# Performance work log

Measured on AMD Instinct MI355X. Metric: run time of the kernel, lower is better.

The kernel has to match this reference:

```python
import jax, jax.numpy as jnp
import numpy as np


def _sig_gram(X, Y, n):
    """Signature-kernel gram matrix via the Goursat PDE recurrence.
    X: (A, M, D), Y: (B, N, D). Returns (A, B) of k(x_a, y_b).
    Recurrence: K[i+1,j+1] = K[i+1,j] + K[i,j+1] + K[i,j]*(inc_ij - 1).
    """
    f = 2 ** n
    # dyadic refinement: increments scaled by 1/2^n, each repeated 2^n times
    dX = jnp.repeat((X[:, 1:] - X[:, :-1]) / f, f, axis=1)  # (A, Mg-1, D)
    dY = jnp.repeat((Y[:, 1:] - Y[:, :-1]) / f, f, axis=1)  # (B, Ng-1, D)
    inc = jnp.einsum('aid,bjd->abij', dX, dY)               # (A, B, Mg-1, Ng-1)
    A, B, _, Ng1 = inc.shape
    ones_col = jnp.ones((A, B, 1), inc.dtype)

    def row_step(K_prev, inc_row):
        # K_prev: row i of the PDE grid, shape (A,B,Ng1+1); inc_row: (A,B,Ng1)
        diag = K_prev[..., :-1] * (inc_row - 1.0)  # K[i,j]*inc - K[i,j]
        up = K_prev[..., 1:]                        # K[i,j+1]

        def col_step(k_left, uv):
            u, d = uv
            k = k_left + u + d
            return k, k

        _, krow = jax.lax.scan(
            col_step,
            jnp.ones((A, B), inc.dtype),
            (jnp.moveaxis(up, -1, 0), jnp.moveaxis(diag, -1, 0)),
        )
        K_new = jnp.concatenate([ones_col, jnp.moveaxis(krow, 0, -1)], axis=-1)
        return K_new, None

    K0 = jnp.ones((A, B, Ng1 + 1), inc.dtype)  # boundary row K[0,:] = 1
    K_last, _ = jax.lax.scan(row_step, K0, jnp.moveaxis(inc, 2, 0))
    return K_last[..., -1]  # K[-1,-1] for every pair


def setup_inputs() -> dict:
    key = jax.random.key(0)
    kx, ky = jax.random.split(key)
    SCALE = 0.05  # keep kernel values in fp32 range (exponential growth)
    X = jax.random.normal(kx, (64, 128, 16), dtype=jnp.float32) * SCALE
    Y = jax.random.normal(ky, (64, 128, 16), dtype=jnp.float32) * SCALE
    return {"X": X, "Y": Y, "n": 0}


def reference(X, Y, n):
    k_xx = _sig_gram(X, X, n)
    k_yy = _sig_gram(Y, Y, n)
    k_xy = _sig_gram(X, Y, n)
    return jnp.mean(k_xx) + jnp.mean(k_yy) - 2.0 * jnp.mean(k_xy)
```

## Files before the change

kernel.cpp:

```cpp
#include <hip/hip_runtime.h>


#define DINC_PER 130048
#define XY_BLOCKS 1024
#define TRI_BLOCKS 544
#define NBT (XY_BLOCKS + 2 * TRI_BLOCKS)
#define NBLOCKS4 2048

template <int C, int RM, int BM, bool BC>
__device__ __forceinline__ float dpp0(float x) {
    return __builtin_bit_cast(float, __builtin_amdgcn_update_dpp(
        0, __builtin_bit_cast(int, x), C, RM, BM, BC));
}

__device__ __forceinline__ float wave_scan_incl(float v) {
    v += dpp0<0x111, 0xf, 0xf, true>(v);
    v += dpp0<0x112, 0xf, 0xf, true>(v);
    v += dpp0<0x114, 0xf, 0xf, true>(v);
    v += dpp0<0x118, 0xf, 0xf, true>(v);
    v += dpp0<0x142, 0xa, 0xf, false>(v);
    v += dpp0<0x143, 0xc, 0xf, false>(v);
    return v;
}

__device__ __forceinline__ float wave_shr1(float x, float oldv) {
    return __builtin_bit_cast(float, __builtin_amdgcn_update_dpp(
        __builtin_bit_cast(int, oldv), __builtin_bit_cast(int, x),
        0x138, 0xf, 0xf, false));
}

__global__ __launch_bounds__(256) void sig_diff(
    const float* __restrict__ X, const float* __restrict__ Y,
    float* __restrict__ dInc, float* __restrict__ out)
{
    if (blockIdx.x == 0 && threadIdx.x == 0) out[0] = 0.0f;
    int i = blockIdx.x * 256 + threadIdx.x;
    if (i >= 65024) return;
    int which = (i >= 32512) ? 1 : 0;
    int j = i - which * 32512;
    int a = j / 508;
    int rq = j - a * 508;
    const float* S = which ? Y : X;
    const float4* p = (const float4*)(S + a * 2048) + rq;
    float4 v0 = p[0], v1 = p[4];
    float4 d;
    d.x = v1.x - v0.x; d.y = v1.y - v0.y;
    d.z = v1.z - v0.z; d.w = v1.w - v0.w;
    ((float4*)dInc)[i] = d;
}

__global__ __launch_bounds__(256, 4) void sig_pde4(
    const float* __restrict__ dInc, float* __restrict__ out)
{
    __shared__ float red[4];
    const int wid  = threadIdx.x >> 6;
    const int lane = threadIdx.x & 63;

    float acc = 0.0f;
    const int nt = (blockIdx.x < (NBT - NBLOCKS4)) ? 2 : 1;

#pragma unroll 1
    for (int it = 0; it < nt; ++it) {
        const int BT = it ? (int)(NBLOCKS4 + blockIdx.x) : (int)blockIdx.x;

        int g, a, b0;
        if (BT < XY_BLOCKS) {
            g = 2; a = BT >> 4; b0 = (BT & 15) << 2;
        } else {
            int t = BT - XY_BLOCKS; g = 0;
            if (t >= TRI_BLOCKS) { t -= TRI_BLOCKS; g = 1; }
            int aa = 0;
            for (;;) { int nb = (67 - aa) >> 2; if (t < nb) break; t -= nb; ++aa; }
            a = aa; b0 = aa + (t << 2);
        }
        const int b = b0 + wid;

        if (g == 2 || b <= 63) {
            const float* dA = (g == 1) ? (dInc + DINC_PER) : dInc;
            const float* dB = (g == 0) ? dInc : (dInc + DINC_PER);
            const float weight = (g == 2) ? (-2.0f / 4096.0f)
                                          : ((a == b ? 1.0f : 2.0f) / 4096.0f);

            float ya[16], yb_[16];
            {
                const float* Qb = dB + b * 2032;
                const int j0 = lane << 1;
                const int j1 = (j0 + 1 < 127) ? j0 + 1 : 126;
                const float4* A4 = (const float4*)(Qb + j0 * 16);
                const float4* B4 = (const float4*)(Qb + j1 * 16);
#pragma unroll
                for (int q = 0; q < 4; ++q) {
                    float4 va = A4[q], vb = B4[q];
                    ya[4*q+0]=va.x;  ya[4*q+1]=va.y;  ya[4*q+2]=va.z;  ya[4*q+3]=va.w;
                    yb_[4*q+0]=vb.x; yb_[4*q+1]=vb.y; yb_[4*q+2]=vb.z; yb_[4*q+3]=vb.w;
                }
            }
#pragma unroll
            for (int d = 0; d < 16; ++d)
                asm volatile("" : "+v"(ya[d]), "+v"(yb_[d]));

            const int abase = __builtin_amdgcn_readfirstlane(a * 2032);
            const float4* Ar = (const float4*)(dA + abase);

            float xr[16], xn[16];
#pragma unroll
            for (int q = 0; q < 4; ++q) {
                float4 v = Ar[q];
                xr[4*q+0]=v.x; xr[4*q+1]=v.y; xr[4*q+2]=v.z; xr[4*q+3]=v.w;
            }

            float g_lo = 1.0f, g_hi = 1.0f;
            const bool last = (lane == 63);

#define SIG_ROW(XROW)                                                       \
            {                                                               \
                float s0=-0.5f, s1=-0.5f, t0=-0.5f, t1=-0.5f;               \
                _Pragma("unroll")                                           \
                for (int d = 0; d < 16; d += 2) {                           \
                    s0 = fmaf(XROW[d],   ya[d],    s0);                     \
                    s1 = fmaf(XROW[d+1], ya[d+1],  s1);                     \
                    t0 = fmaf(XROW[d],   yb_[d],   t0);                     \
                    t1 = fmaf(XROW[d+1], yb_[d+1], t1);                     \
                }                                                           \
                const float i0 = s0 + s1;             \
                const float i1 = t0 + t1;             \
                const float gl = wave_shr1(g_hi, 1.0f);       \
                const float c0 = fmaf(gl, i0, g_lo);                        \
                const float c1 = last ? 0.0f : fmaf(g_lo, i1, g_hi);        \
                const float S  = wave_scan_incl(c0 + c1);                   \
                g_lo = (S - c1) + 1.0f;                                     \
                g_hi = S + 1.0f;                                            \
            }

#pragma unroll 1
            for (int r = 0; r < 126; r += 2) {
#pragma unroll
                for (int q = 0; q < 4; ++q) {
                    float4 v = Ar[4*(r+1)+q];
                    xn[4*q+0]=v.x; xn[4*q+1]=v.y; xn[4*q+2]=v.z; xn[4*q+3]=v.w;
                }
                SIG_ROW(xr)
#pragma unroll
                for (int q = 0; q < 4; ++q) {
                    float4 v = Ar[4*(r+2)+q];
                    xr[4*q+0]=v.x; xr[4*q+1]=v.y; xr[4*q+2]=v.z; xr[4*q+3]=v.w;
                }
                SIG_ROW(xn)
            }
            SIG_ROW(xr)
#undef SIG_ROW

            const float kab = __builtin_bit_cast(float,
                __builtin_amdgcn_readlane(__builtin_bit_cast(int, g_lo), 63));
            acc = fmaf(weight, kab, acc);
        }
    }

    if (lane == 0) red[wid] = acc;
    __syncthreads();
    if (threadIdx.x == 0)
        atomicAdd(out, (red[0] + red[1]) + (red[2] + red[3]));
}

__global__ __launch_bounds__(256) void sig_reduce2(
    const float* __restrict__ v, float* __restrict__ out, int n)
{
    __shared__ float red[256];
    float s = 0.0f;
    for (int i = threadIdx.x; i < n; i += 256) s += v[i];
    red[threadIdx.x] = s;
    __syncthreads();
    for (int st = 128; st > 0; st >>= 1) {
        if (threadIdx.x < st) red[threadIdx.x] += red[threadIdx.x + st];
        __syncthreads();
    }
    if (threadIdx.x == 0) out[0] = red[0];
}

__global__ __launch_bounds__(64) void sig_pde_kernel(
    const float* __restrict__ X, const float* __restrict__ Y,
    float* __restrict__ ws)
{
    __shared__ float Xs[2048];
    const int T = blockIdx.x;
    const int g = T >> 12;
    const int t = T & 4095;
    const int a = t >> 6, b = t & 63;
    const int lane = threadIdx.x;
    if (g < 2 && a > b) { if (lane == 0) ws[T] = 0.0f; return; }
    const float* P = (g == 1) ? Y : X;
    const float* Q = (g == 0) ? X : Y;
    const float weight = (g == 2) ? (-2.0f / 4096.0f)
                                  : ((a == b ? 1.0f : 2.0f) / 4096.0f);
    {
        const float4* Pa = (const float4*)(P + a * 2048);
        float4* Xs4 = (float4*)Xs;
#pragma unroll
        for (int k = 0; k < 8; ++k) Xs4[lane + (k << 6)] = Pa[lane + (k << 6)];
    }
    __syncthreads();
    {
        float tmp[32];
#pragma unroll
        for (int k = 0; k < 32; ++k) {
            int idx = lane + (k << 6);
            tmp[k] = (idx < 2032) ? (Xs[idx + 16] - Xs[idx]) : 0.0f;
        }
        __syncthreads();
#pragma unroll
        for (int k = 0; k < 32; ++k) {
            int idx = lane + (k << 6);
            if (idx < 2032) Xs[idx] = tmp[k];
        }
    }
    __syncthreads();
    float y0[16], y1[16];
    {
        const float* Qb = Q + b * 2048;
        const int r0 = lane << 1;
        const int r2 = (r0 + 2 > 127) ? 127 : (r0 + 2);
        const float4* A4 = (const float4*)(Qb + r0 * 16);
        const float4* B4 = (const float4*)(Qb + (r0 + 1) * 16);
        const float4* C4 = (const float4*)(Qb + r2 * 16);
#pragma unroll
        for (int q = 0; q < 4; ++q) {
            float4 ra = A4[q], rb = B4[q], rc = C4[q];
            y0[4*q+0] = rb.x - ra.x;  y1[4*q+0] = rc.x - rb.x;
            y0[4*q+1] = rb.y - ra.y;  y1[4*q+1] = rc.y - rb.y;
            y0[4*q+2] = rb.z - ra.z;  y1[4*q+2] = rc.z - rb.z;
            y0[4*q+3] = rb.w - ra.w;  y1[4*q+3] = rc.w - rb.w;
        }
    }
    float g_lo = 1.0f, g_hi = 1.0f;
    const bool last = (lane == 63);
    for (int r = 0; r < 127; ++r) {
        const float* xrow = Xs + r * 16;
        float s0 = -0.5f, s1 = -0.5f, t0 = -0.5f, t1 = -0.5f;
#pragma unroll
        for (int d = 0; d < 16; d += 2) {
            s0 = fmaf(xrow[d], y0[d], s0);   s1 = fmaf(xrow[d+1], y0[d+1], s1);
            t0 = fmaf(xrow[d], y1[d], t0);   t1 = fmaf(xrow[d+1], y1[d+1], t1);
        }
        const float i0 = s0 + s1, i1 = t0 + t1;
        const float gl = wave_shr1(g_hi, 1.0f);
        const float c0 = fmaf(gl, i0, g_lo);
        const float c1 = last ? 0.0f : fmaf(g_lo, i1, g_hi);
        const float S = wave_scan_incl(c0 + c1);
        g_lo = (S - c1) + 1.0f;
        g_hi = S + 1.0f;
    }
    const float kab = __builtin_bit_cast(float,
        __builtin_amdgcn_readlane(__builtin_bit_cast(int, g_lo), 63));
    if (lane == 0) ws[T] = weight * kab;
}

extern "C" void kernel_launch(void* const* d_in, const int* in_sizes, int n_in,
                              void* d_out, int out_size, void* d_ws, size_t ws_size,
                              hipStream_t stream) {
    const float* X = (const float*)d_in[0];
    const float* Y = (const float*)d_in[1];
    float* out = (float*)d_out;
    float* ws  = (float*)d_ws;

    const size_t need = (size_t)(2 * DINC_PER) * sizeof(float);
    if (ws_size >= need) {
        sig_diff<<<254, 256, 0, stream>>>(X, Y, ws, out);
        sig_pde4<<<NBLOCKS4, 256, 0, stream>>>(ws, out);
    } else {
        sig_pde_kernel<<<12288, 64, 0, stream>>>(X, Y, ws);
        sig_reduce2<<<1, 256, 0, stream>>>(ws, out, 12288);
    }
}
```

Before: 147.2 us.

## Fuse increment computation into PDE kernel via telescoping dot products

Drops the separate difference pre-pass kernel. The PDE kernel now reads raw X/Y directly: the B-side increments are differenced in registers at load time, and the A-side increments come from telescoping consecutive raw-row dot products (inc = D_{r+1} - D_r). The output is zeroed with a memset, and launch bounds are raised to allow 8 blocks per CU. This removes a kernel launch and a workspace round-trip, in exchange for a different floating-point summation order and a memset launch.

Result: slower. 275.3 us (+87.1%).

```diff
diff --git a/kernel.cpp b/kernel.cpp
--- a/kernel.cpp
+++ b/kernel.cpp
@@ -1,11 +1,10 @@
 #include <hip/hip_runtime.h>
 
 
-#define DINC_PER 130048
 #define XY_BLOCKS 1024
 #define TRI_BLOCKS 544
 #define NBT (XY_BLOCKS + 2 * TRI_BLOCKS)
-#define NBLOCKS4 2048
+#define NBLOCKS6 2048
 
 template <int C, int RM, int BM, bool BC>
 __device__ __forceinline__ float dpp0(float x) {
@@ -29,39 +28,20 @@
         0x138, 0xf, 0xf, false));
 }
 
-__global__ __launch_bounds__(256) void sig_diff(
+__global__ __launch_bounds__(256, 8) void sig_pde6(
     const float* __restrict__ X, const float* __restrict__ Y,
-    float* __restrict__ dInc, float* __restrict__ out)
-{
-    if (blockIdx.x == 0 && threadIdx.x == 0) out[0] = 0.0f;
-    int i = blockIdx.x * 256 + threadIdx.x;
-    if (i >= 65024) return;
-    int which = (i >= 32512) ? 1 : 0;
-    int j = i - which * 32512;
-    int a = j / 508;
-    int rq = j - a * 508;
-    const float* S = which ? Y : X;
-    const float4* p = (const float4*)(S + a * 2048) + rq;
-    float4 v0 = p[0], v1 = p[4];
-    float4 d;
-    d.x = v1.x - v0.x; d.y = v1.y - v0.y;
-    d.z = v1.z - v0.z; d.w = v1.w - v0.w;
-    ((float4*)dInc)[i] = d;
-}
-
-__global__ __launch_bounds__(256, 4) void sig_pde4(
-    const float* __restrict__ dInc, float* __restrict__ out)
+    float* __restrict__ out)
 {
     __shared__ float red[4];
     const int wid  = threadIdx.x >> 6;
     const int lane = threadIdx.x & 63;
 
     float acc = 0.0f;
-    const int nt = (blockIdx.x < (NBT - NBLOCKS4)) ? 2 : 1;
+    const int nt = (blockIdx.x < (NBT - NBLOCKS6)) ? 2 : 1;
 
 #pragma unroll 1
     for (int it = 0; it < nt; ++it) {
-        const int BT = it ? (int)(NBLOCKS4 + blockIdx.x) : (int)blockIdx.x;
+        const int BT = it ? (int)(NBLOCKS6 + blockIdx.x) : (int)blockIdx.x;
 
         int g, a, b0;
         if (BT < XY_BLOCKS) {
@@ -76,37 +56,59 @@
         const int b = b0 + wid;
 
         if (g == 2 || b <= 63) {
-            const float* dA = (g == 1) ? (dInc + DINC_PER) : dInc;
-            const float* dB = (g == 0) ? dInc : (dInc + DINC_PER);
+            const float* A = (g == 1) ? Y : X;
+            const float* Bp = (g == 0) ? X : Y;
             const float weight = (g == 2) ? (-2.0f / 4096.0f)
                                           : ((a == b ? 1.0f : 2.0f) / 4096.0f);
 
             float ya[16], yb_[16];
             {
-                const float* Qb = dB + b * 2032;
+                const float* Qb = Bp + b * 2048;
                 const int j0 = lane << 1;
-                const int j1 = (j0 + 1 < 127) ? j0 + 1 : 126;
-                const float4* A4 = (const float4*)(Qb + j0 * 16);
-                const float4* B4 = (const float4*)(Qb + j1 * 16);
+                const int r2 = (j0 + 2 < 128) ? j0 + 2 : 127;
+                const float4* R0 = (const float4*)(Qb + j0 * 16);
+                const float4* R1 = (const float4*)(Qb + (j0 + 1) * 16);
+                const float4* R2 = (const float4*)(Qb + r2 * 16);
 #pragma unroll
                 for (int q = 0; q < 4; ++q) {
-                    float4 va = A4[q], vb = B4[q];
-                    ya[4*q+0]=va.x;  ya[4*q+1]=va.y;  ya[4*q+2]=va.z;  ya[4*q+3]=va.w;
-                    yb_[4*q+0]=vb.x; yb_[4*q+1]=vb.y; yb_[4*q+2]=vb.z; yb_[4*q+3]=vb.w;
+                    float4 v0 = R0[q], v1 = R1[q], v2 = R2[q];
+                    ya[4*q+0] = v1.x - v0.x;  yb_[4*q+0] = v2.x - v1.x;
+                    ya[4*q+1] = v1.y - v0.y;  yb_[4*q+1] = v2.y - v1.y;
+                    ya[4*q+2] = v1.z - v0.z;  yb_[4*q+2] = v2.z - v1.z;
+                    ya[4*q+3] = v1.w - v0.w;  yb_[4*q+3] = v2.w - v1.w;
                 }
             }
 #pragma unroll
             for (int d = 0; d < 16; ++d)
                 asm volatile("" : "+v"(ya[d]), "+v"(yb_[d]));
 
-            const int abase = __builtin_amdgcn_readfirstlane(a * 2032);
-            const float4* Ar = (const float4*)(dA + abase);
+            const int abase = __builtin_amdgcn_readfirstlane(a * 2048);
+            const float4* Ar = (const float4*)(A + abase);
 
-            float xr[16], xn[16];
+            float xc[16], xn[16];
+            float Es, Et;
+            {
+                float p0[16];
+#pragma unroll
+                for (int q = 0; q < 4; ++q) {
+                    float4 v = Ar[q];
+                    p0[4*q+0]=v.x; p0[4*q+1]=v.y; p0[4*q+2]=v.z; p0[4*q+3]=v.w;
+                }
+                float s0=0.f, s1=0.f, t0=0.f, t1=0.f;
+#pragma unroll
+                for (int d = 0; d < 16; d += 2) {
+                    s0 = fmaf(p0[d],   ya[d],    s0);
+                    s1 = fmaf(p0[d+1], ya[d+1],  s1);
+                    t0 = fmaf(p0[d],   yb_[d],   t0);
+                    t1 = fmaf(p0[d+1], yb_[d+1], t1);
+                }
+                Es = (s0 + s1) + 1.0f;
+                Et = (t0 + t1) + 1.0f;
+            }
 #pragma unroll
             for (int q = 0; q < 4; ++q) {
-                float4 v = Ar[q];
-                xr[4*q+0]=v.x; xr[4*q+1]=v.y; xr[4*q+2]=v.z; xr[4*q+3]=v.w;
+                float4 v = Ar[4 + q];
+                xc[4*q+0]=v.x; xc[4*q+1]=v.y; xc[4*q+2]=v.z; xc[4*q+3]=v.w;
             }
 
             float g_lo = 1.0f, g_hi = 1.0f;
@@ -114,7 +116,7 @@
 
 #define SIG_ROW(XROW)                                                       \
             {                                                               \
-                float s0=-0.5f, s1=-0.5f, t0=-0.5f, t1=-0.5f;               \
+                float s0=0.f, s1=0.f, t0=0.f, t1=0.f;                       \
                 _Pragma("unroll")                                           \
                 for (int d = 0; d < 16; d += 2) {                           \
                     s0 = fmaf(XROW[d],   ya[d],    s0);                     \
@@ -122,8 +124,10 @@
                     t0 = fmaf(XROW[d],   yb_[d],   t0);                     \
                     t1 = fmaf(XROW[d+1], yb_[d+1], t1);                     \
                 }                                                           \
-                const float i0 = s0 + s1;             \
-                const float i1 = t0 + t1;             \
+                const float Ds = s0 + s1, Dt = t0 + t1;                     \
+                const float i0 = Ds - Es;             \
+                const float i1 = Dt - Et;             \
+                Es = Ds + 1.0f;  Et = Dt + 1.0f;                            \
                 const float gl = wave_shr1(g_hi, 1.0f);       \
                 const float c0 = fmaf(gl, i0, g_lo);                        \
                 const float c1 = last ? 0.0f : fmaf(g_lo, i1, g_hi);        \
@@ -136,18 +140,18 @@
             for (int r = 0; r < 126; r += 2) {
 #pragma unroll
                 for (int q = 0; q < 4; ++q) {
-                    float4 v = Ar[4*(r+1)+q];
+                    float4 v = Ar[4*(r+2)+q];
                     xn[4*q+0]=v.x; xn[4*q+1]=v.y; xn[4*q+2]=v.z; xn[4*q+3]=v.w;
                 }
-                SIG_ROW(xr)
+                SIG_ROW(xc)
 #pragma unroll
                 for (int q = 0; q < 4; ++q) {
-                    float4 v = Ar[4*(r+2)+q];
-                    xr[4*q+0]=v.x; xr[4*q+1]=v.y; xr[4*q+2]=v.z; xr[4*q+3]=v.w;
+                    float4 v = Ar[4*(r+3)+q];
+                    xc[4*q+0]=v.x; xc[4*q+1]=v.y; xc[4*q+2]=v.z; xc[4*q+3]=v.w;
                 }
                 SIG_ROW(xn)
             }
-            SIG_ROW(xr)
+            SIG_ROW(xc)
 #undef SIG_ROW
 
             const float kab = __builtin_bit_cast(float,
@@ -162,112 +166,14 @@
         atomicAdd(out, (red[0] + red[1]) + (red[2] + red[3]));
 }
 
-__global__ __launch_bounds__(256) void sig_reduce2(
-    const float* __restrict__ v, float* __restrict__ out, int n)
-{
-    __shared__ float red[256];
-    float s = 0.0f;
-    for (int i = threadIdx.x; i < n; i += 256) s += v[i];
-    red[threadIdx.x] = s;
-    __syncthreads();
-    for (int st = 128; st > 0; st >>= 1) {
-        if (threadIdx.x < st) red[threadIdx.x] += red[threadIdx.x + st];
-        __syncthreads();
-    }
-    if (threadIdx.x == 0) out[0] = red[0];
-}
-
-__global__ __launch_bounds__(64) void sig_pde_kernel(
-    const float* __restrict__ X, const float* __restrict__ Y,
-    float* __restrict__ ws)
-{
-    __shared__ float Xs[2048];
-    const int T = blockIdx.x;
-    const int g = T >> 12;
-    const int t = T & 4095;
-    const int a = t >> 6, b = t & 63;
-    const int lane = threadIdx.x;
-    if (g < 2 && a > b) { if (lane == 0) ws[T] = 0.0f; return; }
-    const float* P = (g == 1) ? Y : X;
-    const float* Q = (g == 0) ? X : Y;
-    const float weight = (g == 2) ? (-2.0f / 4096.0f)
-                                  : ((a == b ? 1.0f : 2.0f) / 4096.0f);
-    {
-        const float4* Pa = (const float4*)(P + a * 2048);
-        float4* Xs4 = (float4*)Xs;
-#pragma unroll
-        for (int k = 0; k < 8; ++k) Xs4[lane + (k << 6)] = Pa[lane + (k << 6)];
-    }
-    __syncthreads();
-    {
-        float tmp[32];
-#pragma unroll
-        for (int k = 0; k < 32; ++k) {
-            int idx = lane + (k << 6);
-            tmp[k] = (idx < 2032) ? (Xs[idx + 16] - Xs[idx]) : 0.0f;
-        }
-        __syncthreads();
-#pragma unroll
-        for (int k = 0; k < 32; ++k) {
-            int idx = lane + (k << 6);
-            if (idx < 2032) Xs[idx] = tmp[k];
-        }
-    }
-    __syncthreads();
-    float y0[16], y1[16];
-    {
-        const float* Qb = Q + b * 2048;
-        const int r0 = lane << 1;
-        const int r2 = (r0 + 2 > 127) ? 127 : (r0 + 2);
-        const float4* A4 = (const float4*)(Qb + r0 * 16);
-        const float4* B4 = (const float4*)(Qb + (r0 + 1) * 16);
-        const float4* C4 = (const float4*)(Qb + r2 * 16);
-#pragma unroll
-        for (int q = 0; q < 4; ++q) {
-            float4 ra = A4[q], rb = B4[q], rc = C4[q];
-            y0[4*q+0] = rb.x - ra.x;  y1[4*q+0] = rc.x - rb.x;
-            y0[4*q+1] = rb.y - ra.y;  y1[4*q+1] = rc.y - rb.y;
-            y0[4*q+2] = rb.z - ra.z;  y1[4*q+2] = rc.z - rb.z;
-            y0[4*q+3] = rb.w - ra.w;  y1[4*q+3] = rc.w - rb.w;
-        }
-    }
-    float g_lo = 1.0f, g_hi = 1.0f;
-    const bool last = (lane == 63);
-    for (int r = 0; r < 127; ++r) {
-        const float* xrow = Xs + r * 16;
-        float s0 = -0.5f, s1 = -0.5f, t0 = -0.5f, t1 = -0.5f;
-#pragma unroll
-        for (int d = 0; d < 16; d += 2) {
-            s0 = fmaf(xrow[d], y0[d], s0);   s1 = fmaf(xrow[d+1], y0[d+1], s1);
-            t0 = fmaf(xrow[d], y1[d], t0);   t1 = fmaf(xrow[d+1], y1[d+1], t1);
-        }
-        const float i0 = s0 + s1, i1 = t0 + t1;
-        const float gl = wave_shr1(g_hi, 1.0f);
-        const float c0 = fmaf(gl, i0, g_lo);
-        const float c1 = last ? 0.0f : fmaf(g_lo, i1, g_hi);
-        const float S = wave_scan_incl(c0 + c1);
-        g_lo = (S - c1) + 1.0f;
-        g_hi = S + 1.0f;
-    }
-    const float kab = __builtin_bit_cast(float,
-        __builtin_amdgcn_readlane(__builtin_bit_cast(int, g_lo), 63));
-    if (lane == 0) ws[T] = weight * kab;
-}
-
 extern "C" void kernel_launch(void* const* d_in, const int* in_sizes, int n_in,
                               void* d_out, int out_size, void* d_ws, size_t ws_size,
                               hipStream_t stream) {
     const float* X = (const float*)d_in[0];
     const float* Y = (const float*)d_in[1];
     float* out = (float*)d_out;
-    float* ws  = (float*)d_ws;
+    (void)d_ws; (void)ws_size;
 
-    const size_t need = (size_t)(2 * DINC_PER) * sizeof(float);
-    if (ws_size >= need) {
-        sig_diff<<<254, 256, 0, stream>>>(X, Y, ws, out);
-        sig_pde4<<<NBLOCKS4, 256, 0, stream>>>(ws, out);
-    } else {
-        sig_pde_kernel<<<12288, 64, 0, stream>>>(X, Y, ws);
-        sig_reduce2<<<1, 256, 0, stream>>>(ws, out, 12288);
-    }
+    hipMemsetAsync(out, 0, sizeof(float), stream);
+    sig_pde6<<<NBLOCKS6, 256, 0, stream>>>(X, Y, out);
 }
```

## Stage X path rows in LDS and launch one block per tile at higher occupancy

Applied to the files above, without the earlier changes.

Each block now stages its shared X path increments (508 float4) into shared memory once, and every wave reads rows from LDS instead of issuing scalar/global loads per row. The persistent two-tile loop is removed: the kernel launches one block per tile (NBT blocks), with launch bounds raised to allow 8 blocks per CU. The manual double-buffered prefetch and the register pinning asm are also dropped. The aim is more waves in flight to hide the serial DPP scan latency. The cost is a block-wide sync, LDS reads on the critical path, and losing the explicit row prefetch.

Result: faster. 134.5 us (-8.6%).

```diff
diff --git a/kernel.cpp b/kernel.cpp
--- a/kernel.cpp
+++ b/kernel.cpp
@@ -1,11 +1,10 @@
 #include <hip/hip_runtime.h>
 
 
-#define DINC_PER 130048
 #define XY_BLOCKS 1024
 #define TRI_BLOCKS 544
 #define NBT (XY_BLOCKS + 2 * TRI_BLOCKS)
-#define NBLOCKS4 2048
+#define DINC_PER 130048
 
 template <int C, int RM, int BM, bool BC>
 __device__ __forceinline__ float dpp0(float x) {
@@ -49,111 +48,89 @@
     ((float4*)dInc)[i] = d;
 }
 
-__global__ __launch_bounds__(256, 4) void sig_pde4(
+__global__ __launch_bounds__(256, 8) void sig_pde8(
     const float* __restrict__ dInc, float* __restrict__ out)
 {
+    __shared__ float4 Xs4[508];
     __shared__ float red[4];
     const int wid  = threadIdx.x >> 6;
     const int lane = threadIdx.x & 63;
+    const int BT   = blockIdx.x;
+
+    int g, a, b0;
+    if (BT < XY_BLOCKS) {
+        g = 2; a = BT >> 4; b0 = (BT & 15) << 2;
+    } else {
+        int t = BT - XY_BLOCKS; g = 0;
+        if (t >= TRI_BLOCKS) { t -= TRI_BLOCKS; g = 1; }
+        int aa = 0;
+        for (;;) { int nb = (67 - aa) >> 2; if (t < nb) break; t -= nb; ++aa; }
+        a = aa; b0 = aa + (t << 2);
+    }
+    const int b = b0 + wid;
+
+    const float* dA = (g == 1) ? (dInc + DINC_PER) : dInc;
+    const float* dB = (g == 0) ? dInc : (dInc + DINC_PER);
+
+    {
+        const float4* Ap = (const float4*)(dA + a * 2032);
+        const int tid = threadIdx.x;
+        Xs4[tid] = Ap[tid];
+        if (tid + 256 < 508) Xs4[tid + 256] = Ap[tid + 256];
+    }
+    __syncthreads();
 
     float acc = 0.0f;
-    const int nt = (blockIdx.x < (NBT - NBLOCKS4)) ? 2 : 1;
+    if (g == 2 || b <= 63) {
+        const float weight = (g == 2) ? (-2.0f / 4096.0f)
+                                      : ((a == b ? 1.0f : 2.0f) / 4096.0f);
+
+        float ya[16], yb_[16];
+        {
+            const float* Qb = dB + b * 2032;
+            const int j0 = lane << 1;
+            const int j1 = (j0 + 1 < 127) ? j0 + 1 : 126;
+            const float4* A4 = (const float4*)(Qb + j0 * 16);
+            const float4* B4 = (const float4*)(Qb + j1 * 16);
+#pragma unroll
+            for (int q = 0; q < 4; ++q) {
+                float4 va = A4[q], vb = B4[q];
+                ya[4*q+0]=va.x;  ya[4*q+1]=va.y;  ya[4*q+2]=va.z;  ya[4*q+3]=va.w;
+                yb_[4*q+0]=vb.x; yb_[4*q+1]=vb.y; yb_[4*q+2]=vb.z; yb_[4*q+3]=vb.w;
+            }
+        }
+
+        float g_lo = 1.0f, g_hi = 1.0f;
+        const bool last = (lane == 63);
 
 #pragma unroll 1
-    for (int it = 0; it < nt; ++it) {
-        const int BT = it ? (int)(NBLOCKS4 + blockIdx.x) : (int)blockIdx.x;
-
-        int g, a, b0;
-        if (BT < XY_BLOCKS) {
-            g = 2; a = BT >> 4; b0 = (BT & 15) << 2;
-        } else {
-            int t = BT - XY_BLOCKS; g = 0;
-            if (t >= TRI_BLOCKS) { t -= TRI_BLOCKS; g = 1; }
-            int aa = 0;
-            for (;;) { int nb = (67 - aa) >> 2; if (t < nb) break; t -= nb; ++aa; }
-            a = aa; b0 = aa + (t << 2);
-        }
-        const int b = b0 + wid;
-
-        if (g == 2 || b <= 63) {
-            const float* dA = (g == 1) ? (dInc + DINC_PER) : dInc;
-            const float* dB = (g == 0) ? dInc : (dInc + DINC_PER);
-            const float weight = (g == 2) ? (-2.0f / 4096.0f)
-                                          : ((a == b ? 1.0f : 2.0f) / 4096.0f);
-
-            float ya[16], yb_[16];
-            {
-                const float* Qb = dB + b * 2032;
-                const int j0 = lane << 1;
-                const int j1 = (j0 + 1 < 127) ? j0 + 1 : 126;
-                const float4* A4 = (const float4*)(Qb + j0 * 16);
-                const float4* B4 = (const float4*)(Qb + j1 * 16);
-#pragma unroll
-                for (int q = 0; q < 4; ++q) {
-                    float4 va = A4[q], vb = B4[q];
-                    ya[4*q+0]=va.x;  ya[4*q+1]=va.y;  ya[4*q+2]=va.z;  ya[4*q+3]=va.w;
-                    yb_[4*q+0]=vb.x; yb_[4*q+1]=vb.y; yb_[4*q+2]=vb.z; yb_[4*q+3]=vb.w;
-                }
-            }
-#pragma unroll
-            for (int d = 0; d < 16; ++d)
-                asm volatile("" : "+v"(ya[d]), "+v"(yb_[d]));
-
-            const int abase = __builtin_amdgcn_readfirstlane(a * 2032);
-            const float4* Ar = (const float4*)(dA + abase);
-
-            float xr[16], xn[16];
+        for (int r = 0; r < 127; ++r) {
+            float xr[16];
 #pragma unroll
             for (int q = 0; q < 4; ++q) {
-                float4 v = Ar[q];
+                float4 v = Xs4[4*r + q];
                 xr[4*q+0]=v.x; xr[4*q+1]=v.y; xr[4*q+2]=v.z; xr[4*q+3]=v.w;
             }
-
-            float g_lo = 1.0f, g_hi = 1.0f;
-            const bool last = (lane == 63);
-
-#define SIG_ROW(XROW)                                                       \
-            {                                                               \
-                float s0=-0.5f, s1=-0.5f, t0=-0.5f, t1=-0.5f;               \
-                _Pragma("unroll")                                           \
-                for (int d = 0; d < 16; d += 2) {                           \
-                    s0 = fmaf(XROW[d],   ya[d],    s0);                     \
-                    s1 = fmaf(XROW[d+1], ya[d+1],  s1);                     \
-                    t0 = fmaf(XROW[d],   yb_[d],   t0);                     \
-                    t1 = fmaf(XROW[d+1], yb_[d+1], t1);                     \
-                }                                                           \
-                const float i0 = s0 + s1;             \
-                const float i1 = t0 + t1;             \
-                const float gl = wave_shr1(g_hi, 1.0f);       \
-                const float c0 = fmaf(gl, i0, g_lo);                        \
-                const float c1 = last ? 0.0f : fmaf(g_lo, i1, g_hi);        \
-                const float S  = wave_scan_incl(c0 + c1);                   \
-                g_lo = (S - c1) + 1.0f;                                     \
-                g_hi = S + 1.0f;                                            \
+            float s0 = -0.5f, s1 = -0.5f, t0 = -0.5f, t1 = -0.5f;
+#pragma unroll
+            for (int d = 0; d < 16; d += 2) {
+                s0 = fmaf(xr[d], ya[d], s0);    s1 = fmaf(xr[d+1], ya[d+1], s1);
+                t0 = fmaf(xr[d], yb_[d], t0);   t1 = fmaf(xr[d+1], yb_[d+1], t1);
             }
-
-#pragma unroll 1
-            for (int r = 0; r < 126; r += 2) {
-#pragma unroll
-                for (int q = 0; q < 4; ++q) {
-                    float4 v = Ar[4*(r+1)+q];
-                    xn[4*q+0]=v.x; xn[4*q+1]=v.y; xn[4*q+2]=v.z; xn[4*q+3]=v.w;
-                }
-                SIG_ROW(xr)
-#pragma unroll
-                for (int q = 0; q < 4; ++q) {
-                    float4 v = Ar[4*(r+2)+q];
-                    xr[4*q+0]=v.x; xr[4*q+1]=v.y; xr[4*q+2]=v.z; xr[4*q+3]=v.w;
-                }
-                SIG_ROW(xn)
-            }
-            SIG_ROW(xr)
-#undef SIG_ROW
-
-            const float kab = __builtin_bit_cast(float,
-                __builtin_amdgcn_readlane(__builtin_bit_cast(int, g_lo), 63));
-            acc = fmaf(weight, kab, acc);
-        }
+            const float i0 = s0 + s1;
+            const float i1 = t0 + t1;
+
+            const float gl = wave_shr1(g_hi, 1.0f);
+            const float c0 = fmaf(gl, i0, g_lo);
+            const float c1 = last ? 0.0f : fmaf(g_lo, i1, g_hi);
+            const float S = wave_scan_incl(c0 + c1);
+            g_lo = (S - c1) + 1.0f;
+            g_hi = S + 1.0f;
+        }
+
+        const float kab = __builtin_bit_cast(float,
+            __builtin_amdgcn_readlane(__builtin_bit_cast(int, g_lo), 63));
+        acc = weight * kab;
     }
 
     if (lane == 0) red[wid] = acc;
@@ -265,7 +242,7 @@
     const size_t need = (size_t)(2 * DINC_PER) * sizeof(float);
     if (ws_size >= need) {
         sig_diff<<<254, 256, 0, stream>>>(X, Y, ws, out);
-        sig_pde4<<<NBLOCKS4, 256, 0, stream>>>(ws, out);
+        sig_pde8<<<NBT, 256, 0, stream>>>(ws, out);
     } else {
         sig_pde_kernel<<<12288, 64, 0, stream>>>(X, Y, ws);
         sig_reduce2<<<1, 256, 0, stream>>>(ws, out, 12288);
```
